# Optimization experiments

Hardware: AMD Instinct MI355X
Metric: run time of the kernel (lower is better)

Reference implementation:

```python
import jax, jax.numpy as jnp
import numpy as np

NUM_BEV_FEATURES = 64
NX, NY, NZ = 512, 512, 1
P_PER_BATCH = 30000
BATCH = 4


def setup_inputs() -> dict:
    key = jax.random.key(0)
    pillar_features = jax.random.normal(key, (BATCH * P_PER_BATCH, NUM_BEV_FEATURES), dtype=jnp.float32)
    # Build coords (batch, z, y, x) with unique (y, x) cells per batch (realistic voxelization)
    rng = np.random.default_rng(0)
    coords_list = []
    for b in range(BATCH):
        flat = rng.choice(NY * NX, size=P_PER_BATCH, replace=False)
        y = flat // NX
        x = flat % NX
        c = np.stack([np.full(P_PER_BATCH, b), np.zeros(P_PER_BATCH, dtype=np.int64), y, x], axis=1)
        coords_list.append(c)
    coords = jnp.asarray(np.concatenate(coords_list, axis=0), dtype=jnp.int64)
    return {"pillar_features": pillar_features, "coords": coords, "batch_size": BATCH}


def reference(pillar_features, coords, batch_size):
    # Fused single-scatter equivalent of the per-batch loop in PointPillarScatter.
    # Per-batch cell index: z + y*nx + x; add batch offset to scatter all at once.
    cell = coords[:, 1] + coords[:, 2] * NX + coords[:, 3]          # [P]
    flat_idx = coords[:, 0] * (NZ * NY * NX) + cell                  # [P]
    grid = jnp.zeros((batch_size * NZ * NY * NX, NUM_BEV_FEATURES), dtype=pillar_features.dtype)
    grid = grid.at[flat_idx].set(pillar_features)                    # [B*ny*nx, C]
    # channels_first output: [B, C*nz, ny, nx]
    out = grid.reshape(batch_size, NY, NX, NUM_BEV_FEATURES)
    return jnp.transpose(out, (0, 3, 1, 2))
```

## Files before the change

### kernel.cpp

```cpp
#include <hip/hip_runtime.h>

#define GNX 512
#define GNY 512
#define GC  64

__global__ void pp_fill_map(int* __restrict__ map, int n) {
    int i = blockIdx.x * blockDim.x + threadIdx.x;
    if (i < n) map[i] = -1;
}

__global__ void pp_scatter_idx(const int* __restrict__ coords,
                               int* __restrict__ map, int P) {
    int p = blockIdx.x * blockDim.x + threadIdx.x;
    if (p >= P) return;
    int b = coords[4 * p + 0];
    int z = coords[4 * p + 1];
    int y = coords[4 * p + 2];
    int x = coords[4 * p + 3];
    int cell = b * (GNY * GNX) + z + y * GNX + x;
    map[cell] = p;
}

__global__ void pp_gather_out(const float* __restrict__ feat,
                              const int* __restrict__ map,
                              float4* __restrict__ out, int n4) {
    int tid = blockIdx.x * blockDim.x + threadIdx.x;
    if (tid >= n4) return;
    int e = tid << 2;
    int x    = e & (GNX - 1);
    int rest = e >> 9;
    int y    = rest & (GNY - 1);
    int bc   = rest >> 9;
    int c    = bc & (GC - 1);
    int b    = bc >> 6;
    int cellbase = (b << 18) + (y << 9) + x;
    int4 m = *(const int4*)(map + cellbase);
    float4 v;
    v.x = (m.x >= 0) ? feat[(m.x << 6) + c] : 0.0f;
    v.y = (m.y >= 0) ? feat[(m.y << 6) + c] : 0.0f;
    v.z = (m.z >= 0) ? feat[(m.z << 6) + c] : 0.0f;
    v.w = (m.w >= 0) ? feat[(m.w << 6) + c] : 0.0f;
    out[tid] = v;
}

extern "C" void kernel_launch(void* const* d_in, const int* in_sizes, int n_in,
                              void* d_out, int out_size, void* d_ws, size_t ws_size,
                              hipStream_t stream) {
    const float* feat   = (const float*)d_in[0];
    const int*   coords = (const int*)d_in[1];
    int P = in_sizes[1] / 4;
    int B = out_size / (GC * GNY * GNX);
    int* map = (int*)d_ws;
    int mapN = B * GNY * GNX;

    pp_fill_map<<<(mapN + 255) / 256, 256, 0, stream>>>(map, mapN);

    pp_scatter_idx<<<(P + 255) / 256, 256, 0, stream>>>(coords, map, P);

    int n4 = out_size / 4;
    pp_gather_out<<<(n4 + 255) / 256, 256, 0, stream>>>(feat, map, (float4*)d_out, n4);
}
```

Baseline: 307.0 us.

## Gather 16 channels per thread with float4 feature loads and in-register transpose

The gather kernel now has each thread handle 4 adjacent x cells and a group of 16 channels, with blockIdx.y selecting the channel group. It reads each valid pillar's 16 contiguous channels as four float4 loads instead of one scalar load per channel. It then transposes in registers and writes 16 float4 stores to the channel-first output. This cuts the map reads and the scattered scalar feature loads. The cost is higher register pressure and fewer threads.

Result: no change. 301.7 us (-1.7%).

```diff
diff --git a/kernel.cpp b/kernel.cpp
--- a/kernel.cpp
+++ b/kernel.cpp
@@ -3,6 +3,8 @@
 #define GNX 512
 #define GNY 512
 #define GC  64
+
+#define COMP(v, t) ((t) == 0 ? (v).x : (t) == 1 ? (v).y : (t) == 2 ? (v).z : (v).w)
 
 __global__ void pp_fill_map(int* __restrict__ map, int n) {
     int i = blockIdx.x * blockDim.x + threadIdx.x;
@@ -17,30 +19,55 @@
     int z = coords[4 * p + 1];
     int y = coords[4 * p + 2];
     int x = coords[4 * p + 3];
-    int cell = b * (GNY * GNX) + z + y * GNX + x;
-    map[cell] = p;
+    map[b * (GNY * GNX) + z + y * GNX + x] = p;
 }
 
-__global__ void pp_gather_out(const float* __restrict__ feat,
-                              const int* __restrict__ map,
-                              float4* __restrict__ out, int n4) {
-    int tid = blockIdx.x * blockDim.x + threadIdx.x;
-    if (tid >= n4) return;
-    int e = tid << 2;
-    int x    = e & (GNX - 1);
-    int rest = e >> 9;
-    int y    = rest & (GNY - 1);
-    int bc   = rest >> 9;
-    int c    = bc & (GC - 1);
-    int b    = bc >> 6;
-    int cellbase = (b << 18) + (y << 9) + x;
+__global__ void __launch_bounds__(256) pp_gather_out(
+        const float* __restrict__ feat, const int* __restrict__ map,
+        float* __restrict__ out, int nquad) {
+    int q  = blockIdx.x * blockDim.x + threadIdx.x;
+    if (q >= nquad) return;
+    int cg = blockIdx.y;
+
+    int x4 = q & (GNX / 4 - 1);
+    int y  = (q >> 7) & (GNY - 1);
+    int b  = q >> 16;
+
+    int cellbase = (b << 18) + (y << 9) + (x4 << 2);
     int4 m = *(const int4*)(map + cellbase);
-    float4 v;
-    v.x = (m.x >= 0) ? feat[(m.x << 6) + c] : 0.0f;
-    v.y = (m.y >= 0) ? feat[(m.y << 6) + c] : 0.0f;
-    v.z = (m.z >= 0) ? feat[(m.z << 6) + c] : 0.0f;
-    v.w = (m.w >= 0) ? feat[(m.w << 6) + c] : 0.0f;
-    out[tid] = v;
+
+    float4 fr[4][4];
+#pragma unroll
+    for (int j = 0; j < 4; ++j)
+#pragma unroll
+        for (int k = 0; k < 4; ++k)
+            fr[j][k] = make_float4(0.f, 0.f, 0.f, 0.f);
+
+    {
+        const int pj[4] = { m.x, m.y, m.z, m.w };
+#pragma unroll
+        for (int j = 0; j < 4; ++j) {
+            if (pj[j] >= 0) {
+                const float4* fp = (const float4*)(feat + (pj[j] << 6) + (cg << 4));
+                fr[j][0] = fp[0];
+                fr[j][1] = fp[1];
+                fr[j][2] = fp[2];
+                fr[j][3] = fp[3];
+            }
+        }
+    }
+
+    int rowoff = (y << 9) + (x4 << 2);
+    float* obase = out + (((b << 6) + (cg << 4)) << 18) + rowoff;
+#pragma unroll
+    for (int k = 0; k < 4; ++k) {
+#pragma unroll
+        for (int t = 0; t < 4; ++t) {
+            float4 v = make_float4(COMP(fr[0][k], t), COMP(fr[1][k], t),
+                                   COMP(fr[2][k], t), COMP(fr[3][k], t));
+            *(float4*)(obase + ((k * 4 + t) << 18)) = v;
+        }
+    }
 }
 
 extern "C" void kernel_launch(void* const* d_in, const int* in_sizes, int n_in,
@@ -54,9 +81,9 @@
     int mapN = B * GNY * GNX;
 
     pp_fill_map<<<(mapN + 255) / 256, 256, 0, stream>>>(map, mapN);
-
     pp_scatter_idx<<<(P + 255) / 256, 256, 0, stream>>>(coords, map, P);
 
-    int n4 = out_size / 4;
-    pp_gather_out<<<(n4 + 255) / 256, 256, 0, stream>>>(feat, map, (float4*)d_out, n4);
+    int nquad = B * GNY * (GNX / 4);
+    dim3 grid((nquad + 255) / 256, GC / 16, 1);
+    pp_gather_out<<<grid, 256, 0, stream>>>(feat, map, (float*)d_out, nquad);
 }
```
